# Performance work log

Hardware: AMD Instinct MI355X
Metric: run time of the kernel (lower is better)

## Reference

```python
import jax, jax.numpy as jnp
import numpy as np

B, L, H = 16, 512, 1024
HEADS, HEAD_SIZE = 12, 64
NEG = 1e12


def sinusoidal_position_embedding(seq_len, output_dim):
    pos = jnp.arange(seq_len, dtype=jnp.float32)[:, None]
    idx = jnp.arange(output_dim // 2, dtype=jnp.float32)
    freqs = pos * jnp.power(10000.0, -2.0 * idx / output_dim)  # [L, D/2]
    emb = jnp.stack([jnp.sin(freqs), jnp.cos(freqs)], axis=-1)  # [L, D/2, 2]
    return emb.reshape(seq_len, output_dim)  # interleaved sin/cos, [L, D]


def setup_inputs() -> dict:
    key = jax.random.key(0)
    k1, k2, k3 = jax.random.split(key, 3)
    inputs = jax.random.normal(k1, (B, L, H), dtype=jnp.float32)
    mask = jnp.ones((B, L), dtype=jnp.int32)
    W = jax.random.normal(k2, (H, HEADS * HEAD_SIZE * 2), dtype=jnp.float32) / np.sqrt(H)
    b = jax.random.normal(k3, (HEADS * HEAD_SIZE * 2,), dtype=jnp.float32) * 0.01
    pos_emb = sinusoidal_position_embedding(L, HEAD_SIZE)  # [L, HEAD_SIZE]
    return {"inputs": inputs, "mask": mask, "W": W, "b": b, "pos_emb": pos_emb}


def rotate_half_interleaved(x):
    # stack([-x[..., 1::2], x[..., ::2]], -1).reshape(x.shape)
    x2 = jnp.stack([-x[..., 1::2], x[..., ::2]], axis=-1)
    return x2.reshape(x.shape)


def reference(inputs, mask, W, b, pos_emb):
    bsz, seq_len, _ = inputs.shape
    d = pos_emb.shape[-1]
    heads = W.shape[1] // (2 * d)
    out = inputs @ W + b                       # [B, L, heads*2d]
    out = out.reshape(bsz, seq_len, heads, 2 * d)
    qw, kw = out[..., :d], out[..., d:]        # [B, L, heads, d]
    cos_pos = jnp.repeat(pos_emb[:, 1::2], 2, axis=-1)[None, :, None, :]  # [1,L,1,d]
    sin_pos = jnp.repeat(pos_emb[:, 0::2], 2, axis=-1)[None, :, None, :]
    qw = qw * cos_pos + rotate_half_interleaved(qw) * sin_pos
    kw = kw * cos_pos + rotate_half_interleaved(kw) * sin_pos
    logits = jnp.einsum('bmhd,bnhd->bhmn', qw, kw)  # [B, heads, L, L]
    pad = mask.astype(logits.dtype)[:, None, None, :] * mask.astype(logits.dtype)[:, None, :, None]
    # torch code: expand of mask[:,None,None,:] -> applies along last axis only;
    # replicate exactly: pad_mask broadcasts mask over the query axis.
    pad_mask = jnp.broadcast_to(mask.astype(logits.dtype)[:, None, None, :], logits.shape)
    logits = logits * pad_mask - (1.0 - pad_mask) * NEG
    tril = jnp.tril(jnp.ones((seq_len, seq_len), dtype=logits.dtype), -1)
    logits = logits - tril[None, None, :, :] * NEG
    return logits / jnp.sqrt(jnp.array(d, dtype=logits.dtype))
```

## Files before the change

kernel.cpp:

```cpp
#include <hip/hip_runtime.h>

#define BB 16
#define LL 512
#define HH 1024
#define HEADS 12
#define DD 64
#define N1 1536
#define M1 8192
#define NEGC 1e12f

typedef short bf16x8 __attribute__((ext_vector_type(8)));
typedef float f32x4 __attribute__((ext_vector_type(4)));

__device__ __forceinline__ unsigned short f2bf(float f) {
    union { float f; unsigned int u; } v; v.f = f;
    unsigned int u = v.u;
    return (unsigned short)((u + 0x7fffu + ((u >> 16) & 1u)) >> 16);
}

__global__ __launch_bounds__(256) void k_conv_x(const float* __restrict__ X,
                                                unsigned short* __restrict__ Xb,
                                                int n4) {
    int i = blockIdx.x * 256 + threadIdx.x;
    if (i >= n4) return;
    float4 v = ((const float4*)X)[i];
    ushort4 o;
    o.x = f2bf(v.x); o.y = f2bf(v.y); o.z = f2bf(v.z); o.w = f2bf(v.w);
    ((ushort4*)Xb)[i] = o;
}

__global__ __launch_bounds__(256) void k_trans_w(const float* __restrict__ W,
                                                 unsigned short* __restrict__ Wt) {
    __shared__ float tile[32][33];
    int n0 = blockIdx.x * 32;
    int k0 = blockIdx.y * 32;
    int tx = threadIdx.x;
    int ty = threadIdx.y;
#pragma unroll
    for (int i = 0; i < 4; i++) {
        int k = ty + i * 8;
        tile[k][tx] = W[(size_t)(k0 + k) * N1 + n0 + tx];
    }
    __syncthreads();
#pragma unroll
    for (int i = 0; i < 4; i++) {
        int n = ty + i * 8;
        Wt[(size_t)(n0 + n) * HH + k0 + tx] = f2bf(tile[tx][n]);
    }
}

__global__ __launch_bounds__(256) void k_gemm1_rope(
    const unsigned short* __restrict__ Xb,
    const unsigned short* __restrict__ Wt,
    const float* __restrict__ bias,
    const float* __restrict__ pe,
    unsigned short* __restrict__ Qr,
    unsigned short* __restrict__ Kr)
{
    __shared__ __align__(16) unsigned short As[64 * 40];
    __shared__ __align__(16) unsigned short Bs[64 * 40];
    int m0 = blockIdx.y * 64;
    int n0 = blockIdx.x * 64;
    int tid = threadIdx.x;
    int w  = tid >> 6;
    int ln = tid & 63;
    int lq = ln >> 4;
    int lm = ln & 15;
    int mw = (w & 1) * 32;
    int nw = (w >> 1) * 32;

    int srow = tid >> 2;
    int scol = (tid & 3) * 8;

    f32x4 acc[2][2] = {};

    for (int kk = 0; kk < HH; kk += 32) {
        uint4 av = *(const uint4*)&Xb[(size_t)(m0 + srow) * HH + kk + scol];
        uint4 bv = *(const uint4*)&Wt[(size_t)(n0 + srow) * HH + kk + scol];
        *(uint4*)&As[srow * 40 + scol] = av;
        *(uint4*)&Bs[srow * 40 + scol] = bv;
        __syncthreads();
        bf16x8 af0 = *(const bf16x8*)&As[(mw + lm) * 40 + lq * 8];
        bf16x8 af1 = *(const bf16x8*)&As[(mw + 16 + lm) * 40 + lq * 8];
        bf16x8 bf0 = *(const bf16x8*)&Bs[(nw + lm) * 40 + lq * 8];
        bf16x8 bf1 = *(const bf16x8*)&Bs[(nw + 16 + lm) * 40 + lq * 8];
        acc[0][0] = __builtin_amdgcn_mfma_f32_16x16x32_bf16(af0, bf0, acc[0][0], 0, 0, 0);
        acc[0][1] = __builtin_amdgcn_mfma_f32_16x16x32_bf16(af0, bf1, acc[0][1], 0, 0, 0);
        acc[1][0] = __builtin_amdgcn_mfma_f32_16x16x32_bf16(af1, bf0, acc[1][0], 0, 0, 0);
        acc[1][1] = __builtin_amdgcn_mfma_f32_16x16x32_bf16(af1, bf1, acc[1][1], 0, 0, 0);
        __syncthreads();
    }

#pragma unroll
    for (int nt = 0; nt < 2; nt++) {
        int n = n0 + nw + nt * 16 + lm;
        float bv = bias[n];
        int h = n >> 7;
        int c = n & 127;
        int j = c & 63;
        int ii = j >> 1;
        bool isK = (c >= 64);
#pragma unroll
        for (int mt = 0; mt < 2; mt++) {
#pragma unroll
            for (int r = 0; r < 4; r++) {
                int m = m0 + mw + mt * 16 + lq * 4 + r;
                int l = m & (LL - 1);
                int bidx = m >> 9;
                float v = acc[mt][nt][r] + bv;
                float vp = __shfl_xor(v, 1, 64);
                float sv = pe[l * 64 + 2 * ii];
                float cv = pe[l * 64 + 2 * ii + 1];
                float o = (j & 1) ? (v * cv + vp * sv) : (v * cv - vp * sv);
                unsigned short ob = f2bf(o);
                size_t idx = ((size_t)(bidx * HEADS + h) * LL + l) * DD + j;
                if (isK) Kr[idx] = ob; else Qr[idx] = ob;
            }
        }
    }
}

__global__ __launch_bounds__(256) void k_gemm2(
    const unsigned short* __restrict__ Qr,
    const unsigned short* __restrict__ Kr,
    const int* __restrict__ mask,
    float* __restrict__ out)
{
    __shared__ __align__(16) unsigned short Qs[64 * 72];
    __shared__ __align__(16) unsigned short Ks[64 * 72];
    int bh = blockIdx.z;
    int b  = bh / HEADS;
    int n0 = blockIdx.x * 64;
    int m0 = blockIdx.y * 64;
    int tid = threadIdx.x;
    int w  = tid >> 6;
    int ln = tid & 63;
    int lq = ln >> 4;
    int lm = ln & 15;
    int mw = (w & 1) * 32;
    int nw = (w >> 1) * 32;

    const unsigned short* Qb = Qr + (size_t)bh * LL * DD;
    const unsigned short* Kb = Kr + (size_t)bh * LL * DD;

    int srow = tid >> 3;
    int scol = (tid & 7) * 8;
#pragma unroll
    for (int p = 0; p < 2; p++) {
        int row = srow + p * 32;
        *(uint4*)&Qs[row * 72 + scol] = *(const uint4*)&Qb[(size_t)(m0 + row) * DD + scol];
        *(uint4*)&Ks[row * 72 + scol] = *(const uint4*)&Kb[(size_t)(n0 + row) * DD + scol];
    }
    __syncthreads();

    f32x4 acc[2][2] = {};
#pragma unroll
    for (int kk = 0; kk < 64; kk += 32) {
        bf16x8 a0 = *(const bf16x8*)&Qs[(mw + lm) * 72 + kk + lq * 8];
        bf16x8 a1 = *(const bf16x8*)&Qs[(mw + 16 + lm) * 72 + kk + lq * 8];
        bf16x8 b0 = *(const bf16x8*)&Ks[(nw + lm) * 72 + kk + lq * 8];
        bf16x8 b1 = *(const bf16x8*)&Ks[(nw + 16 + lm) * 72 + kk + lq * 8];
        acc[0][0] = __builtin_amdgcn_mfma_f32_16x16x32_bf16(a0, b0, acc[0][0], 0, 0, 0);
        acc[0][1] = __builtin_amdgcn_mfma_f32_16x16x32_bf16(a0, b1, acc[0][1], 0, 0, 0);
        acc[1][0] = __builtin_amdgcn_mfma_f32_16x16x32_bf16(a1, b0, acc[1][0], 0, 0, 0);
        acc[1][1] = __builtin_amdgcn_mfma_f32_16x16x32_bf16(a1, b1, acc[1][1], 0, 0, 0);
    }

#pragma unroll
    for (int nt = 0; nt < 2; nt++) {
        int n = n0 + nw + nt * 16 + lm;
        float pm = (float)mask[b * LL + n];
        float negn = (1.0f - pm) * NEGC;
#pragma unroll
        for (int mt = 0; mt < 2; mt++) {
#pragma unroll
            for (int r = 0; r < 4; r++) {
                int m = m0 + mw + mt * 16 + lq * 4 + r;
                float dot = acc[mt][nt][r];
                float val = (dot * pm - negn - (n < m ? NEGC : 0.0f)) * 0.125f;
                out[((size_t)bh * LL + m) * LL + n] = val;
            }
        }
    }
}

extern "C" void kernel_launch(void* const* d_in, const int* in_sizes, int n_in,
                              void* d_out, int out_size, void* d_ws, size_t ws_size,
                              hipStream_t stream) {
    const float* X    = (const float*)d_in[0];
    const int*   mask = (const int*)d_in[1];
    const float* W    = (const float*)d_in[2];
    const float* bias = (const float*)d_in[3];
    const float* pe   = (const float*)d_in[4];
    float* out = (float*)d_out;

    char* ws = (char*)d_ws;
    unsigned short* Xb = (unsigned short*)ws;
    unsigned short* Wt = (unsigned short*)(ws + 16777216);
    unsigned short* Qr = (unsigned short*)(ws + 16777216 + 3145728);
    unsigned short* Kr = Qr + (size_t)BB * HEADS * LL * DD;

    k_conv_x<<<dim3((M1 * HH / 4 + 255) / 256), dim3(256), 0, stream>>>(X, Xb, M1 * HH / 4);
    k_trans_w<<<dim3(N1 / 32, HH / 32), dim3(32, 8), 0, stream>>>(W, Wt);
    k_gemm1_rope<<<dim3(N1 / 64, M1 / 64), dim3(256), 0, stream>>>(Xb, Wt, bias, pe, Qr, Kr);
    k_gemm2<<<dim3(LL / 64, LL / 64, BB * HEADS), dim3(256), 0, stream>>>(Qr, Kr, mask, out);
}
```

Baseline: 324.1 us.

## Enlarge GEMM1 tiles with direct global-to-LDS loads, vectorize GEMM2 output stores

GEMM1 moves from 64x64 to 128x128 block tiles, with a 4x4 MFMA tile per wave. Operands are now staged through global_load_lds, which writes straight to shared memory and skips the register round trip. GEMM2 swaps the MFMA operand order so each lane holds four consecutive columns, allowing float4 stores to the large fp32 logits output and int4 mask loads. The bigger tiles raise register pressure and cut the GEMM1 grid to 768 blocks, and the unpadded LDS layout may cause bank conflicts.

```diff
diff --git a/kernel.cpp b/kernel.cpp
--- a/kernel.cpp
+++ b/kernel.cpp
@@ -11,6 +11,13 @@
 
 typedef short bf16x8 __attribute__((ext_vector_type(8)));
 typedef float f32x4 __attribute__((ext_vector_type(4)));
+
+typedef const __attribute__((address_space(1))) unsigned int glob_u32;
+typedef __attribute__((address_space(3))) unsigned int lds_u32;
+
+__device__ __forceinline__ void gl_lds16(const unsigned short* g, unsigned short* l) {
+    __builtin_amdgcn_global_load_lds((glob_u32*)g, (lds_u32*)l, 16, 0, 0);
+}
 
 __device__ __forceinline__ unsigned short f2bf(float f) {
     union { float f; unsigned int u; } v; v.f = f;
@@ -57,64 +64,78 @@
     unsigned short* __restrict__ Qr,
     unsigned short* __restrict__ Kr)
 {
-    __shared__ __align__(16) unsigned short As[64 * 40];
-    __shared__ __align__(16) unsigned short Bs[64 * 40];
-    int m0 = blockIdx.y * 64;
-    int n0 = blockIdx.x * 64;
+    __shared__ __align__(16) unsigned short As[128 * 32];
+    __shared__ __align__(16) unsigned short Bs[128 * 32];
+    int m0 = blockIdx.y * 128;
+    int n0 = blockIdx.x * 128;
     int tid = threadIdx.x;
     int w  = tid >> 6;
     int ln = tid & 63;
     int lq = ln >> 4;
     int lm = ln & 15;
-    int mw = (w & 1) * 32;
-    int nw = (w >> 1) * 32;
-
-    int srow = tid >> 2;
-    int scol = (tid & 3) * 8;
-
-    f32x4 acc[2][2] = {};
+    int wm = (w & 1) * 64;
+    int wn = (w >> 1) * 64;
+
+    int lrow = ln >> 2;
+    int lcol = (ln & 3) * 8;
+    const unsigned short* ga0 = &Xb[(size_t)(m0 + w * 32 + lrow) * HH + lcol];
+    const unsigned short* ga1 = ga0 + (size_t)16 * HH;
+    const unsigned short* gb0 = &Wt[(size_t)(n0 + w * 32 + lrow) * HH + lcol];
+    const unsigned short* gb1 = gb0 + (size_t)16 * HH;
+    unsigned short* la0 = &As[(w * 32) * 32];
+    unsigned short* la1 = la0 + 16 * 32;
+    unsigned short* lb0 = &Bs[(w * 32) * 32];
+    unsigned short* lb1 = lb0 + 16 * 32;
+
+    const unsigned short* pa = &As[(wm + lm) * 32];
+    const unsigned short* pb = &Bs[(wn + lm) * 32];
+
+    f32x4 acc[4][4] = {};
 
     for (int kk = 0; kk < HH; kk += 32) {
-        uint4 av = *(const uint4*)&Xb[(size_t)(m0 + srow) * HH + kk + scol];
-        uint4 bv = *(const uint4*)&Wt[(size_t)(n0 + srow) * HH + kk + scol];
-        *(uint4*)&As[srow * 40 + scol] = av;
-        *(uint4*)&Bs[srow * 40 + scol] = bv;
+        gl_lds16(ga0 + kk, la0);
+        gl_lds16(ga1 + kk, la1);
+        gl_lds16(gb0 + kk, lb0);
+        gl_lds16(gb1 + kk, lb1);
         __syncthreads();
-        bf16x8 af0 = *(const bf16x8*)&As[(mw + lm) * 40 + lq * 8];
-        bf16x8 af1 = *(const bf16x8*)&As[(mw + 16 + lm) * 40 + lq * 8];
-        bf16x8 bf0 = *(const bf16x8*)&Bs[(nw + lm) * 40 + lq * 8];
-        bf16x8 bf1 = *(const bf16x8*)&Bs[(nw + 16 + lm) * 40 + lq * 8];
-        acc[0][0] = __builtin_amdgcn_mfma_f32_16x16x32_bf16(af0, bf0, acc[0][0], 0, 0, 0);
-        acc[0][1] = __builtin_amdgcn_mfma_f32_16x16x32_bf16(af0, bf1, acc[0][1], 0, 0, 0);
-        acc[1][0] = __builtin_amdgcn_mfma_f32_16x16x32_bf16(af1, bf0, acc[1][0], 0, 0, 0);
-        acc[1][1] = __builtin_amdgcn_mfma_f32_16x16x32_bf16(af1, bf1, acc[1][1], 0, 0, 0);
+
+        bf16x8 af[4], bf[4];
+#pragma unroll
+        for (int t = 0; t < 4; t++) {
+            af[t] = *(const bf16x8*)&pa[t * 16 * 32 + lq * 8];
+            bf[t] = *(const bf16x8*)&pb[t * 16 * 32 + lq * 8];
+        }
+#pragma unroll
+        for (int ti = 0; ti < 4; ti++)
+#pragma unroll
+            for (int tj = 0; tj < 4; tj++)
+                acc[ti][tj] = __builtin_amdgcn_mfma_f32_16x16x32_bf16(af[ti], bf[tj], acc[ti][tj], 0, 0, 0);
         __syncthreads();
     }
 
 #pragma unroll
-    for (int nt = 0; nt < 2; nt++) {
-        int n = n0 + nw + nt * 16 + lm;
+    for (int tj = 0; tj < 4; tj++) {
+        int n = n0 + wn + tj * 16 + lm;
         float bv = bias[n];
         int h = n >> 7;
         int c = n & 127;
         int j = c & 63;
         int ii = j >> 1;
         bool isK = (c >= 64);
-#pragma unroll
-        for (int mt = 0; mt < 2; mt++) {
+        unsigned short* dst = isK ? Kr : Qr;
+#pragma unroll
+        for (int ti = 0; ti < 4; ti++) {
 #pragma unroll
             for (int r = 0; r < 4; r++) {
-                int m = m0 + mw + mt * 16 + lq * 4 + r;
+                int m = m0 + wm + ti * 16 + lq * 4 + r;
                 int l = m & (LL - 1);
                 int bidx = m >> 9;
-                float v = acc[mt][nt][r] + bv;
+                float v = acc[ti][tj][r] + bv;
                 float vp = __shfl_xor(v, 1, 64);
-                float sv = pe[l * 64 + 2 * ii];
-                float cv = pe[l * 64 + 2 * ii + 1];
-                float o = (j & 1) ? (v * cv + vp * sv) : (v * cv - vp * sv);
-                unsigned short ob = f2bf(o);
+                float2 sc = *(const float2*)&pe[l * 64 + 2 * ii];
+                float o = (j & 1) ? (v * sc.y + vp * sc.x) : (v * sc.y - vp * sc.x);
                 size_t idx = ((size_t)(bidx * HEADS + h) * LL + l) * DD + j;
-                if (isK) Kr[idx] = ob; else Qr[idx] = ob;
+                dst[idx] = f2bf(o);
             }
         }
     }
@@ -156,30 +177,41 @@
     f32x4 acc[2][2] = {};
 #pragma unroll
     for (int kk = 0; kk < 64; kk += 32) {
-        bf16x8 a0 = *(const bf16x8*)&Qs[(mw + lm) * 72 + kk + lq * 8];
-        bf16x8 a1 = *(const bf16x8*)&Qs[(mw + 16 + lm) * 72 + kk + lq * 8];
-        bf16x8 b0 = *(const bf16x8*)&Ks[(nw + lm) * 72 + kk + lq * 8];
-        bf16x8 b1 = *(const bf16x8*)&Ks[(nw + 16 + lm) * 72 + kk + lq * 8];
-        acc[0][0] = __builtin_amdgcn_mfma_f32_16x16x32_bf16(a0, b0, acc[0][0], 0, 0, 0);
-        acc[0][1] = __builtin_amdgcn_mfma_f32_16x16x32_bf16(a0, b1, acc[0][1], 0, 0, 0);
-        acc[1][0] = __builtin_amdgcn_mfma_f32_16x16x32_bf16(a1, b0, acc[1][0], 0, 0, 0);
-        acc[1][1] = __builtin_amdgcn_mfma_f32_16x16x32_bf16(a1, b1, acc[1][1], 0, 0, 0);
-    }
-
-#pragma unroll
-    for (int nt = 0; nt < 2; nt++) {
-        int n = n0 + nw + nt * 16 + lm;
-        float pm = (float)mask[b * LL + n];
-        float negn = (1.0f - pm) * NEGC;
-#pragma unroll
-        for (int mt = 0; mt < 2; mt++) {
-#pragma unroll
-            for (int r = 0; r < 4; r++) {
-                int m = m0 + mw + mt * 16 + lq * 4 + r;
-                float dot = acc[mt][nt][r];
-                float val = (dot * pm - negn - (n < m ? NEGC : 0.0f)) * 0.125f;
-                out[((size_t)bh * LL + m) * LL + n] = val;
-            }
+        bf16x8 q0 = *(const bf16x8*)&Qs[(mw + lm) * 72 + kk + lq * 8];
+        bf16x8 q1 = *(const bf16x8*)&Qs[(mw + 16 + lm) * 72 + kk + lq * 8];
+        bf16x8 k0 = *(const bf16x8*)&Ks[(nw + lm) * 72 + kk + lq * 8];
+        bf16x8 k1 = *(const bf16x8*)&Ks[(nw + 16 + lm) * 72 + kk + lq * 8];
+        acc[0][0] = __builtin_amdgcn_mfma_f32_16x16x32_bf16(k0, q0, acc[0][0], 0, 0, 0);
+        acc[0][1] = __builtin_amdgcn_mfma_f32_16x16x32_bf16(k1, q0, acc[0][1], 0, 0, 0);
+        acc[1][0] = __builtin_amdgcn_mfma_f32_16x16x32_bf16(k0, q1, acc[1][0], 0, 0, 0);
+        acc[1][1] = __builtin_amdgcn_mfma_f32_16x16x32_bf16(k1, q1, acc[1][1], 0, 0, 0);
+    }
+
+#pragma unroll
+    for (int tm = 0; tm < 2; tm++) {
+        int m = m0 + mw + tm * 16 + lm;
+#pragma unroll
+        for (int tn = 0; tn < 2; tn++) {
+            int nb = n0 + nw + tn * 16 + lq * 4;
+            int4 mv = *(const int4*)&mask[b * LL + nb];
+            float4 val;
+            {
+                float pm = (float)mv.x; int n = nb;
+                val.x = (acc[tm][tn][0] * pm - (1.0f - pm) * NEGC - (n < m ? NEGC : 0.0f)) * 0.125f;
+            }
+            {
+                float pm = (float)mv.y; int n = nb + 1;
+                val.y = (acc[tm][tn][1] * pm - (1.0f - pm) * NEGC - (n < m ? NEGC : 0.0f)) * 0.125f;
+            }
+            {
+                float pm = (float)mv.z; int n = nb + 2;
+                val.z = (acc[tm][tn][2] * pm - (1.0f - pm) * NEGC - (n < m ? NEGC : 0.0f)) * 0.125f;
+            }
+            {
+                float pm = (float)mv.w; int n = nb + 3;
+                val.w = (acc[tm][tn][3] * pm - (1.0f - pm) * NEGC - (n < m ? NEGC : 0.0f)) * 0.125f;
+            }
+            *(float4*)&out[((size_t)bh * LL + m) * LL + nb] = val;
         }
     }
 }
@@ -202,6 +234,6 @@
 
     k_conv_x<<<dim3((M1 * HH / 4 + 255) / 256), dim3(256), 0, stream>>>(X, Xb, M1 * HH / 4);
     k_trans_w<<<dim3(N1 / 32, HH / 32), dim3(32, 8), 0, stream>>>(W, Wt);
-    k_gemm1_rope<<<dim3(N1 / 64, M1 / 64), dim3(256), 0, stream>>>(Xb, Wt, bias, pe, Qr, Kr);
+    k_gemm1_rope<<<dim3(N1 / 128, M1 / 128), dim3(256), 0, stream>>>(Xb, Wt, bias, pe, Qr, Kr);
     k_gemm2<<<dim3(LL / 64, LL / 64, BB * HEADS), dim3(256), 0, stream>>>(Qr, Kr, mask, out);
 }
```

After: 327.2 us. No clear change (+1.0%).
